# Optimization experiments

Hardware: AMD Instinct MI355X
Metric: run time of the kernel (lower is better)

## Reference

```python
import jax, jax.numpy as jnp
import numpy as np

N_NODES = 100000
N_EDGES = 3200000
N_GRAPHS = 1024


def gcn_conv(x, src, dst, W, b):
    """GCNConv with symmetric normalization and implicit self-loops.
    x: [N, Fin], src/dst: [E] int, W: [Fin, Fout], b: [Fout]."""
    n = x.shape[0]
    h = x @ W  # [N, Fout]
    # degree including self-loop
    deg = jnp.zeros((n,), h.dtype).at[dst].add(1.0) + 1.0
    dinv = deg ** -0.5
    norm = dinv[src] * dinv[dst]  # [E]
    agg = jnp.zeros_like(h).at[dst].add(norm[:, None] * h[src])
    # self-loop contribution: dinv[i]^2 * h[i]
    agg = agg + (dinv * dinv)[:, None] * h
    return agg + b


def setup_inputs() -> dict:
    key = jax.random.key(0)
    ks = jax.random.split(key, 12)
    F, H = 128, 64
    x = jax.random.normal(ks[0], (N_NODES, F), jnp.float32)
    edge_index = jax.random.randint(ks[1], (2, N_EDGES), 0, N_NODES, jnp.int32)
    batch = jnp.sort(jax.random.randint(ks[2], (N_NODES,), 0, N_GRAPHS, jnp.int32))
    def w(k, i, o):
        return jax.random.normal(k, (i, o), jnp.float32) * (1.0 / np.sqrt(i))
    return {
        "x": x, "edge_index": edge_index, "batch": batch,
        "W1": w(ks[3], F, H), "b1": jnp.zeros((H,), jnp.float32),
        "W2": w(ks[4], H, H), "b2": jnp.zeros((H,), jnp.float32),
        "W3": w(ks[5], H, H // 2), "b3": jnp.zeros((H // 2,), jnp.float32),
        "Wc1": w(ks[6], H // 2, H // 4), "bc1": jnp.zeros((H // 4,), jnp.float32),
        "Wc2": w(ks[7], H // 4, 16), "bc2": jnp.zeros((16,), jnp.float32),
    }


def reference(x, edge_index, batch, W1, b1, W2, b2, W3, b3, Wc1, bc1, Wc2, bc2):
    src, dst = edge_index[0], edge_index[1]
    h = jax.nn.relu(gcn_conv(x, src, dst, W1, b1))
    h = jax.nn.relu(gcn_conv(h, src, dst, W2, b2))
    h = jax.nn.relu(gcn_conv(h, src, dst, W3, b3))
    # global mean pool over graphs (dropout is identity at inference)
    sums = jax.ops.segment_sum(h, batch, num_segments=N_GRAPHS)
    counts = jax.ops.segment_sum(jnp.ones((h.shape[0],), h.dtype), batch,
                                 num_segments=N_GRAPHS)
    pooled = sums / jnp.maximum(counts, 1.0)[:, None]  # [G, 32]
    z = jax.nn.relu(pooled @ Wc1 + bc1)
    logits = z @ Wc2 + bc2
    return jax.nn.log_softmax(logits, axis=-1)
```

## Files before the change

### kernel.cpp

```cpp
#include <hip/hip_runtime.h>
#include <hip/hip_bf16.h>
#include <hip/hip_fp16.h>
#include <math.h>


constexpr int BSHIFT = 8;
constexpr int BMASK  = 255;
constexpr int BCAP   = 10240;
constexpr int EPB    = 4096;

__global__ __launch_bounds__(512) void partition_kernel(const int* __restrict__ src,
    const int* __restrict__ dst, int* __restrict__ bucket_cnt,
    unsigned* __restrict__ part, unsigned* __restrict__ runmap,
    int E, int nbuckets, int nblk) {
  __shared__ int lcnt[512];
  __shared__ int lscan[512];
  __shared__ int lcur[512];
  __shared__ unsigned spay[EPB];
  const int t = threadIdx.x;
  const int blk = blockIdx.x;
  const int base = blk * EPB;
  const int lim = min(EPB, E - base);
  int s[8], d[8];
#pragma unroll
  for (int j = 0; j < 8; ++j) {
    int idx = base + j * 512 + t;
    if (idx < E) { s[j] = src[idx]; d[j] = dst[idx]; } else d[j] = -1;
  }
  lcnt[t] = 0;
  __syncthreads();
#pragma unroll
  for (int j = 0; j < 8; ++j)
    if (d[j] >= 0) atomicAdd(&lcnt[d[j] >> BSHIFT], 1);
  __syncthreads();
  const int myv = lcnt[t];
  lscan[t] = myv;
  __syncthreads();
  for (int dd = 1; dd < 512; dd <<= 1) {
    int v = 0;
    if (t >= dd) v = lscan[t - dd];
    __syncthreads();
    if (t >= dd) lscan[t] += v;
    __syncthreads();
  }
  const int excl = lscan[t] - myv;
  if (t < nbuckets) {
    runmap[(size_t)t * nblk + blk] = (unsigned)excl | ((unsigned)myv << 16);
    if (myv > 0) atomicAdd(&bucket_cnt[t], myv);
  }
  lcur[t] = excl;
  __syncthreads();
#pragma unroll
  for (int j = 0; j < 8; ++j) {
    if (d[j] >= 0) {
      int b = d[j] >> BSHIFT;
      int pos = atomicAdd(&lcur[b], 1);
      spay[pos] = ((unsigned)(d[j] & BMASK) << 17) | (unsigned)s[j];
    }
  }
  __syncthreads();
#pragma unroll
  for (int j = 0; j < 8; ++j) {
    int i = j * 512 + t;
    if (i < lim) part[base + i] = spay[i];
  }
}

__global__ __launch_bounds__(256) void scan_buckets_kernel(const int* __restrict__ cnt,
    int* __restrict__ base, int nb) {
  __shared__ int sh[512];
  const int t = threadIdx.x;
  sh[t] = (t < nb) ? cnt[t] : 0;
  sh[t + 256] = (t + 256 < nb) ? cnt[t + 256] : 0;
  __syncthreads();
  for (int d = 1; d < 512; d <<= 1) {
    int v0 = 0, v1 = 0;
    if (t >= d) v0 = sh[t - d];
    if (t + 256 >= d) v1 = sh[t + 256 - d];
    __syncthreads();
    if (t >= d) sh[t] += v0;
    if (t + 256 >= d) sh[t + 256] += v1;
    __syncthreads();
  }
  if (t < nb) base[t] = (t == 0) ? 0 : sh[t - 1];
  if (t + 256 < nb) base[t + 256] = sh[t + 255];
}

__global__ __launch_bounds__(512) void fill_bucket_kernel(
    const unsigned* __restrict__ part, const unsigned* __restrict__ runmap,
    const int* __restrict__ bucket_base, int* __restrict__ offs,
    float* __restrict__ dinv, int* __restrict__ csr, int N, int E, int nblk) {
  __shared__ int lwin[BCAP];
  __shared__ unsigned rrun[1024];
  __shared__ int ldeg[256];
  __shared__ int lscan[512];
  const int b = blockIdx.x;
  const int t = threadIdx.x;
  const int nb0 = b << BSHIFT;
  const int nn = min(1 << BSHIFT, N - nb0);
  const int wbase = bucket_base[b];
  for (int i = t; i < nblk; i += 512) rrun[i] = runmap[(size_t)b * nblk + i];
  if (t < 256) ldeg[t] = 0;
  __syncthreads();
  for (int r = t; r < nblk; r += 512) {
    unsigned v = rrun[r];
    int start = (int)(v & 0xFFFFu), cnt = (int)(v >> 16);
    const unsigned* p = part + (size_t)r * EPB + start;
    for (int k = 0; k < cnt; ++k) atomicAdd(&ldeg[p[k] >> 17], 1);
  }
  __syncthreads();
  const int myv = (t < 256) ? ldeg[t] : 0;
  lscan[t] = myv;
  __syncthreads();
  for (int d = 1; d < 256; d <<= 1) {
    int v = 0;
    if (t >= d && t < 256) v = lscan[t - d];
    __syncthreads();
    if (t >= d && t < 256) lscan[t] += v;
    __syncthreads();
  }
  const int excl = lscan[t] - myv;
  if (t < nn) {
    offs[nb0 + t] = wbase + excl;
    dinv[nb0 + t] = 1.0f / sqrtf((float)(myv + 1));
  }
  if (t == 0 && nb0 + nn == N) offs[N] = E;
  if (t < 256) ldeg[t] = excl;
  __syncthreads();
  for (int r = t; r < nblk; r += 512) {
    unsigned v = rrun[r];
    int start = (int)(v & 0xFFFFu), cnt = (int)(v >> 16);
    const unsigned* p = part + (size_t)r * EPB + start;
    for (int k = 0; k < cnt; ++k) {
      unsigned e = p[k];
      int pos = atomicAdd(&ldeg[e >> 17], 1);
      if (pos < BCAP) lwin[pos] = (int)(e & 0x1FFFF);
    }
  }
  __syncthreads();
  const int total = min(lscan[255], BCAP);
  for (int i = t; i < total; i += 512) csr[wbase + i] = lwin[i];
}

template <int K, int M>
__global__ __launch_bounds__(256) void gemm_kernel(const float* __restrict__ X,
    const float* __restrict__ W, __half* __restrict__ Y, int n) {
  constexpr int RPB = 32;
  constexpr int XST = K + 4;
  constexpr int MC = M / 16;
  __shared__ __align__(16) float Ws[K * M];
  __shared__ __align__(16) float Xs[RPB * XST];
  const int tid = threadIdx.x;
  const int row0 = blockIdx.x * RPB;
  for (int i = tid * 4; i < K * M; i += 1024)
    *reinterpret_cast<float4*>(&Ws[i]) = *reinterpret_cast<const float4*>(&W[i]);
  for (int i = tid * 4; i < RPB * K; i += 1024) {
    int r = i / K, k = i - r * K;
    int gr = row0 + r;
    float4 v = make_float4(0.f, 0.f, 0.f, 0.f);
    if (gr < n) v = *reinterpret_cast<const float4*>(&X[(size_t)gr * K + k]);
    *reinterpret_cast<float4*>(&Xs[r * XST + k]) = v;
  }
  __syncthreads();
  const int rt = tid & 15;
  const int c = tid >> 4;
  float acc[2][MC];
#pragma unroll
  for (int rr = 0; rr < 2; ++rr)
#pragma unroll
    for (int j = 0; j < MC; ++j) acc[rr][j] = 0.f;
  for (int k4 = 0; k4 < K; k4 += 4) {
    float4 xv[2];
#pragma unroll
    for (int rr = 0; rr < 2; ++rr)
      xv[rr] = *reinterpret_cast<const float4*>(&Xs[(rt + 16 * rr) * XST + k4]);
    const float* xf0 = reinterpret_cast<const float*>(&xv[0]);
    const float* xf1 = reinterpret_cast<const float*>(&xv[1]);
#pragma unroll
    for (int kk = 0; kk < 4; ++kk) {
      float w[MC];
#pragma unroll
      for (int j = 0; j < MC; ++j) w[j] = Ws[(k4 + kk) * M + c * MC + j];
      float x0 = xf0[kk], x1 = xf1[kk];
#pragma unroll
      for (int j = 0; j < MC; ++j) {
        acc[0][j] += x0 * w[j];
        acc[1][j] += x1 * w[j];
      }
    }
  }
#pragma unroll
  for (int rr = 0; rr < 2; ++rr) {
    int gr = row0 + rt + 16 * rr;
    if (gr < n) {
#pragma unroll
      for (int j = 0; j < MC; ++j)
        Y[(size_t)gr * M + c * MC + j] = __float2half(acc[rr][j]);
    }
  }
}

__device__ inline void h8_acc(uint4 r, float w, float* acc) {
  const __half2* hp = reinterpret_cast<const __half2*>(&r);
#pragma unroll
  for (int q = 0; q < 4; ++q) {
    float2 f = __half22float2(hp[q]);
    acc[2 * q]     += w * f.x;
    acc[2 * q + 1] += w * f.y;
  }
}

template <int FOUT>
__global__ __launch_bounds__(256) void agg_gemm_kernel(
    const __half* __restrict__ h, const int* __restrict__ offs,
    const int* __restrict__ csr, const float* __restrict__ dinv,
    const float* __restrict__ bias, const float* __restrict__ W,
    __half* __restrict__ y, int n) {
  constexpr int FIN = 64;
  constexpr int XST = FIN + 4;
  __shared__ float Xs[32 * XST];
  __shared__ __align__(16) float Wls[FIN * FOUT];
  const int t = threadIdx.x;
  for (int i = t * 4; i < FIN * FOUT; i += 1024)
    *reinterpret_cast<float4*>(&Wls[i]) = *reinterpret_cast<const float4*>(&W[i]);
  const int r = t >> 3;
  const int node = blockIdx.x * 32 + r;
  const int fl = (t & 7) * 8;
  float acc[8];
#pragma unroll
  for (int j = 0; j < 8; ++j) acc[j] = 0.f;
  if (node < n) {
    const int e0 = offs[node], e1 = offs[node + 1];
    const float di = dinv[node];
    {
      uint4 rr = *reinterpret_cast<const uint4*>(h + (size_t)node * FIN + fl);
      h8_acc(rr, di * di, acc);
    }
    int e = e0;
    for (; e + 4 <= e1; e += 4) {
      int sidx[4];
      float wv[4];
      uint4 rv[4];
#pragma unroll
      for (int u = 0; u < 4; ++u) sidx[u] = csr[e + u];
#pragma unroll
      for (int u = 0; u < 4; ++u) wv[u] = di * dinv[sidx[u]];
#pragma unroll
      for (int u = 0; u < 4; ++u)
        rv[u] = *reinterpret_cast<const uint4*>(h + (size_t)sidx[u] * FIN + fl);
#pragma unroll
      for (int u = 0; u < 4; ++u) h8_acc(rv[u], wv[u], acc);
    }
    for (; e < e1; ++e) {
      int s = csr[e];
      uint4 rr = *reinterpret_cast<const uint4*>(h + (size_t)s * FIN + fl);
      h8_acc(rr, di * dinv[s], acc);
    }
#pragma unroll
    for (int j = 0; j < 8; ++j)
      Xs[r * XST + fl + j] = fmaxf(acc[j] + bias[fl + j], 0.f);
  }
  __syncthreads();
  constexpr int CPT = FOUT / 8;
  const int c0 = (t & 7) * CPT;
  float a2[CPT];
#pragma unroll
  for (int j = 0; j < CPT; ++j) a2[j] = 0.f;
  for (int k = 0; k < FIN; ++k) {
    float xv = Xs[r * XST + k];
    const float4 wa = *reinterpret_cast<const float4*>(&Wls[k * FOUT + c0]);
    a2[0] += xv * wa.x; a2[1] += xv * wa.y;
    a2[2] += xv * wa.z; a2[3] += xv * wa.w;
    if constexpr (CPT == 8) {
      const float4 wb = *reinterpret_cast<const float4*>(&Wls[k * FOUT + c0 + 4]);
      a2[4] += xv * wb.x; a2[5] += xv * wb.y;
      a2[6] += xv * wb.z; a2[7] += xv * wb.w;
    }
  }
  if (node < n) {
    union { __half hh[CPT]; uint4 u4; uint2 u2; } cv;
#pragma unroll
    for (int j = 0; j < CPT; ++j) cv.hh[j] = __float2half(a2[j]);
    if constexpr (CPT == 8)
      *reinterpret_cast<uint4*>(y + (size_t)node * FOUT + c0) = cv.u4;
    else
      *reinterpret_cast<uint2*>(y + (size_t)node * FOUT + c0) = cv.u2;
  }
}

__global__ __launch_bounds__(256) void agg_pool_kernel(const __half* __restrict__ h,
    const int* __restrict__ offs, const int* __restrict__ csr,
    const float* __restrict__ dinv, const float* __restrict__ bias,
    const int* __restrict__ batch, float* __restrict__ gsum, int n, int G) {
  constexpr int F = 32;
  constexpr int GCAP = 8;
  __shared__ float lg[GCAP * F];
  const int t = threadIdx.x;
  const int node0 = blockIdx.x * 64;
  const int node = node0 + (t >> 2);
  const int fl = (t & 3) * 8;
  for (int i = t; i < GCAP * F; i += 256) lg[i] = 0.f;
  __syncthreads();
  const int g0 = batch[node0 < n ? node0 : (n - 1)];
  if (node < n) {
    const int e0 = offs[node], e1 = offs[node + 1];
    const float di = dinv[node];
    float acc[8];
#pragma unroll
    for (int j = 0; j < 8; ++j) acc[j] = 0.f;
    {
      uint4 rr = *reinterpret_cast<const uint4*>(h + (size_t)node * F + fl);
      h8_acc(rr, di * di, acc);
    }
    int e = e0;
    for (; e + 4 <= e1; e += 4) {
      int sidx[4];
      float wv[4];
      uint4 rv[4];
#pragma unroll
      for (int u = 0; u < 4; ++u) sidx[u] = csr[e + u];
#pragma unroll
      for (int u = 0; u < 4; ++u) wv[u] = di * dinv[sidx[u]];
#pragma unroll
      for (int u = 0; u < 4; ++u)
        rv[u] = *reinterpret_cast<const uint4*>(h + (size_t)sidx[u] * F + fl);
#pragma unroll
      for (int u = 0; u < 4; ++u) h8_acc(rv[u], wv[u], acc);
    }
    for (; e < e1; ++e) {
      int s = csr[e];
      uint4 rr = *reinterpret_cast<const uint4*>(h + (size_t)s * F + fl);
      h8_acc(rr, di * dinv[s], acc);
    }
    const int rel = batch[node] - g0;
    if (rel < GCAP) {
#pragma unroll
      for (int j = 0; j < 8; ++j)
        atomicAdd(&lg[rel * F + fl + j], fmaxf(acc[j] + bias[fl + j], 0.f));
    } else {
      float* gp = gsum + (size_t)batch[node] * F + fl;
#pragma unroll
      for (int j = 0; j < 8; ++j)
        atomicAdd(&gp[j], fmaxf(acc[j] + bias[fl + j], 0.f));
    }
  }
  __syncthreads();
  for (int i = t; i < GCAP * F; i += 256) {
    float v = lg[i];
    int gi = g0 * F + i;
    if (v != 0.f && gi < G * F) atomicAdd(&gsum[gi], v);
  }
}

__global__ __launch_bounds__(256) void head_kernel(const float* __restrict__ gsum,
    const int* __restrict__ batch, const float* __restrict__ Wc1,
    const float* __restrict__ bc1, const float* __restrict__ Wc2,
    const float* __restrict__ bc2, float* __restrict__ out, int n, int G) {
  int g = blockIdx.x * blockDim.x + threadIdx.x;
  if (g >= G) return;
  int lo = 0, hi = n;
  while (lo < hi) { int m = (lo + hi) >> 1; if (batch[m] < g) lo = m + 1; else hi = m; }
  const int s0 = lo;
  lo = s0; hi = n;
  while (lo < hi) { int m = (lo + hi) >> 1; if (batch[m] < g + 1) lo = m + 1; else hi = m; }
  const float inv = 1.0f / fmaxf((float)(lo - s0), 1.0f);
  float p[32];
#pragma unroll
  for (int k = 0; k < 32; ++k) p[k] = gsum[g * 32 + k] * inv;
  float z[16];
#pragma unroll
  for (int j = 0; j < 16; ++j) {
    float a = bc1[j];
#pragma unroll
    for (int k = 0; k < 32; ++k) a += p[k] * Wc1[k * 16 + j];
    z[j] = fmaxf(a, 0.f);
  }
  float lg[16];
  float m = -1e30f;
#pragma unroll
  for (int j = 0; j < 16; ++j) {
    float a = bc2[j];
#pragma unroll
    for (int k = 0; k < 16; ++k) a += z[k] * Wc2[k * 16 + j];
    lg[j] = a;
    m = fmaxf(m, a);
  }
  float ssum = 0.f;
#pragma unroll
  for (int j = 0; j < 16; ++j) ssum += expf(lg[j] - m);
  float lse = logf(ssum);
#pragma unroll
  for (int j = 0; j < 16; ++j) out[g * 16 + j] = lg[j] - m - lse;
}

extern "C" void kernel_launch(void* const* d_in, const int* in_sizes, int n_in,
                              void* d_out, int out_size, void* d_ws, size_t ws_size,
                              hipStream_t stream) {
  const float* x   = (const float*)d_in[0];
  const int*   ei  = (const int*)d_in[1];
  const int*   batch = (const int*)d_in[2];
  const float* W1 = (const float*)d_in[3];
  const float* b1 = (const float*)d_in[4];
  const float* W2 = (const float*)d_in[5];
  const float* b2 = (const float*)d_in[6];
  const float* W3 = (const float*)d_in[7];
  const float* b3 = (const float*)d_in[8];
  const float* Wc1 = (const float*)d_in[9];
  const float* bc1 = (const float*)d_in[10];
  const float* Wc2 = (const float*)d_in[11];
  const float* bc2 = (const float*)d_in[12];

  const int N = in_sizes[2];
  const int E = in_sizes[1] / 2;
  const int G = out_size / 16;
  const int* src = ei;
  const int* dst = ei + E;
  const int nbuckets = (N + ((1 << BSHIFT) - 1)) >> BSHIFT;
  const int nblk = (E + EPB - 1) / EPB;

  char* ws = (char*)d_ws;
  size_t off = 0;
  auto alloc = [&](size_t bytes) -> void* {
    void* p = ws + off;
    off += (bytes + 511) & ~(size_t)511;
    return p;
  };
  int*   offs   = (int*)alloc(((size_t)N + 1) * 4);
  float* dinv   = (float*)alloc((size_t)N * 4);
  int*   bucket_cnt  = (int*)alloc(2048);
  int*   bucket_base = (int*)alloc(2048);
  unsigned* runmap = (unsigned*)alloc((size_t)nbuckets * nblk * 4);
  int*   csr    = (int*)alloc((size_t)E * 4);
  __half* hbufA = (__half*)alloc((size_t)N * 64 * 2);
  __half* hbufB = (__half*)alloc((size_t)N * 64 * 2);
  __half* hbufC = (__half*)alloc((size_t)N * 32 * 2);
  float* gsum   = (float*)alloc((size_t)G * 32 * 4);
  unsigned* part = (unsigned*)hbufA;
  (void)ws_size; (void)n_in;

  hipMemsetAsync(bucket_cnt, 0, (size_t)nbuckets * 4, stream);
  hipMemsetAsync(gsum, 0, (size_t)G * 32 * 4, stream);
  partition_kernel<<<nblk, 512, 0, stream>>>(src, dst, bucket_cnt, part, runmap,
                                             E, nbuckets, nblk);
  scan_buckets_kernel<<<1, 256, 0, stream>>>(bucket_cnt, bucket_base, nbuckets);
  fill_bucket_kernel<<<nbuckets, 512, 0, stream>>>(part, runmap, bucket_base,
                                                   offs, dinv, csr, N, E, nblk);

  gemm_kernel<128, 64><<<(N + 31) / 32, 256, 0, stream>>>(x, W1, hbufA, N);
  agg_gemm_kernel<64><<<(N + 31) / 32, 256, 0, stream>>>(hbufA, offs, csr, dinv,
                                                         b1, W2, hbufB, N);
  agg_gemm_kernel<32><<<(N + 31) / 32, 256, 0, stream>>>(hbufB, offs, csr, dinv,
                                                         b2, W3, hbufC, N);
  agg_pool_kernel<<<(N + 63) / 64, 256, 0, stream>>>(hbufC, offs, csr, dinv,
                                                     b3, batch, gsum, N, G);
  head_kernel<<<(G + 255) / 256, 256, 0, stream>>>(gsum, batch, Wc1, bc1,
                                                   Wc2, bc2, (float*)d_out, N, G);
}
```

Measured before the change: 337.5 us.

## Stage bucket edges in shared memory once in fill_bucket_kernel

The fill kernel now scans the per-run counts, copies every bucket edge from the partition buffer into a shared-memory buffer once, and runs both the degree count and the CSR scatter from that buffer with all threads striding over edges. Before, it read the global partition runs twice, one thread per run walking serially. The CSR is now written straight to global at the atomic position instead of through a shared staging window, so writes are less coalesced. The kernel also assumes nblk is at most 1024 and uses rsqrtf for dinv.

```diff
diff --git a/kernel.cpp b/kernel.cpp
--- a/kernel.cpp
+++ b/kernel.cpp
@@ -88,10 +88,11 @@
 
 __global__ __launch_bounds__(512) void fill_bucket_kernel(
     const unsigned* __restrict__ part, const unsigned* __restrict__ runmap,
-    const int* __restrict__ bucket_base, int* __restrict__ offs,
-    float* __restrict__ dinv, int* __restrict__ csr, int N, int E, int nblk) {
-  __shared__ int lwin[BCAP];
-  __shared__ unsigned rrun[1024];
+    const int* __restrict__ bucket_cnt, const int* __restrict__ bucket_base,
+    int* __restrict__ offs, float* __restrict__ dinv, int* __restrict__ csr,
+    int N, int E, int nblk) {
+  __shared__ unsigned ebuf[BCAP];
+  __shared__ int rsh[1024];
   __shared__ int ldeg[256];
   __shared__ int lscan[512];
   const int b = blockIdx.x;
@@ -99,15 +100,36 @@
   const int nb0 = b << BSHIFT;
   const int nn = min(1 << BSHIFT, N - nb0);
   const int wbase = bucket_base[b];
-  for (int i = t; i < nblk; i += 512) rrun[i] = runmap[(size_t)b * nblk + i];
+  const int cnt = min(bucket_cnt[b], BCAP);
+  const unsigned r0 = (t < nblk) ? runmap[(size_t)b * nblk + t] : 0u;
+  const unsigned r1 = (t + 512 < nblk) ? runmap[(size_t)b * nblk + t + 512] : 0u;
+  const int c0 = (int)(r0 >> 16), c1 = (int)(r1 >> 16);
+  rsh[t] = c0; rsh[t + 512] = c1;
   if (t < 256) ldeg[t] = 0;
   __syncthreads();
-  for (int r = t; r < nblk; r += 512) {
-    unsigned v = rrun[r];
-    int start = (int)(v & 0xFFFFu), cnt = (int)(v >> 16);
-    const unsigned* p = part + (size_t)r * EPB + start;
-    for (int k = 0; k < cnt; ++k) atomicAdd(&ldeg[p[k] >> 17], 1);
-  }
+  for (int dd = 1; dd < 1024; dd <<= 1) {
+    int x0 = 0, x1 = 0;
+    if (t >= dd) x0 = rsh[t - dd];
+    x1 = rsh[t + 512 - dd];
+    __syncthreads();
+    if (t >= dd) rsh[t] += x0;
+    rsh[t + 512] += x1;
+    __syncthreads();
+  }
+  {
+    int rb = rsh[t] - c0;
+    if (c0 > 0) {
+      const unsigned* p = part + (size_t)t * EPB + (r0 & 0xFFFFu);
+      for (int k = 0; k < c0; ++k) { int o = rb + k; if (o < BCAP) ebuf[o] = p[k]; }
+    }
+    int rb1 = rsh[t + 512] - c1;
+    if (c1 > 0) {
+      const unsigned* p = part + (size_t)(t + 512) * EPB + (r1 & 0xFFFFu);
+      for (int k = 0; k < c1; ++k) { int o = rb1 + k; if (o < BCAP) ebuf[o] = p[k]; }
+    }
+  }
+  __syncthreads();
+  for (int i = t; i < cnt; i += 512) atomicAdd(&ldeg[ebuf[i] >> 17], 1);
   __syncthreads();
   const int myv = (t < 256) ? ldeg[t] : 0;
   lscan[t] = myv;
@@ -122,24 +144,16 @@
   const int excl = lscan[t] - myv;
   if (t < nn) {
     offs[nb0 + t] = wbase + excl;
-    dinv[nb0 + t] = 1.0f / sqrtf((float)(myv + 1));
+    dinv[nb0 + t] = rsqrtf((float)(myv + 1));
   }
   if (t == 0 && nb0 + nn == N) offs[N] = E;
   if (t < 256) ldeg[t] = excl;
   __syncthreads();
-  for (int r = t; r < nblk; r += 512) {
-    unsigned v = rrun[r];
-    int start = (int)(v & 0xFFFFu), cnt = (int)(v >> 16);
-    const unsigned* p = part + (size_t)r * EPB + start;
-    for (int k = 0; k < cnt; ++k) {
-      unsigned e = p[k];
-      int pos = atomicAdd(&ldeg[e >> 17], 1);
-      if (pos < BCAP) lwin[pos] = (int)(e & 0x1FFFF);
-    }
-  }
-  __syncthreads();
-  const int total = min(lscan[255], BCAP);
-  for (int i = t; i < total; i += 512) csr[wbase + i] = lwin[i];
+  for (int i = t; i < cnt; i += 512) {
+    unsigned v = ebuf[i];
+    int pos = atomicAdd(&ldeg[v >> 17], 1);
+    if (pos < BCAP) csr[wbase + pos] = (int)(v & 0x1FFFF);
+  }
 }
 
 template <int K, int M>
@@ -443,8 +457,9 @@
   partition_kernel<<<nblk, 512, 0, stream>>>(src, dst, bucket_cnt, part, runmap,
                                              E, nbuckets, nblk);
   scan_buckets_kernel<<<1, 256, 0, stream>>>(bucket_cnt, bucket_base, nbuckets);
-  fill_bucket_kernel<<<nbuckets, 512, 0, stream>>>(part, runmap, bucket_base,
-                                                   offs, dinv, csr, N, E, nblk);
+  fill_bucket_kernel<<<nbuckets, 512, 0, stream>>>(part, runmap, bucket_cnt,
+                                                   bucket_base, offs, dinv, csr,
+                                                   N, E, nblk);
 
   gemm_kernel<128, 64><<<(N + 31) / 32, 256, 0, stream>>>(x, W1, hbufA, N);
   agg_gemm_kernel<64><<<(N + 31) / 32, 256, 0, stream>>>(hbufA, offs, csr, dinv,
```

Result: no change. 335.7 us (-0.5%).
